# Performance work log

Hardware: AMD Instinct MI355X
Metric: run time of the kernel (lower is better)

Reference implementation:

```python
import jax, jax.numpy as jnp
import numpy as np

D_MODEL = 1024
H = 16
D_K = D_MODEL // H
D_FF = 4096
EPS = 1e-6


def setup_inputs() -> dict:
    key = jax.random.key(0)
    ks = jax.random.split(key, 12)
    B, S = 8, 1024
    s = 0.02
    inp = {
        "x": jax.random.normal(ks[0], (B, S, D_MODEL), dtype=jnp.float32),
        "src_mask": jnp.ones((B, 1, 1, S), dtype=jnp.int32),
        "wq": jax.random.normal(ks[1], (D_MODEL, D_MODEL), dtype=jnp.float32) * s,
        "bq": jnp.zeros((D_MODEL,), jnp.float32),
        "wk": jax.random.normal(ks[2], (D_MODEL, D_MODEL), dtype=jnp.float32) * s,
        "bk": jnp.zeros((D_MODEL,), jnp.float32),
        "wv": jax.random.normal(ks[3], (D_MODEL, D_MODEL), dtype=jnp.float32) * s,
        "bv": jnp.zeros((D_MODEL,), jnp.float32),
        "wo": jax.random.normal(ks[4], (D_MODEL, D_MODEL), dtype=jnp.float32) * s,
        "bo": jnp.zeros((D_MODEL,), jnp.float32),
        "w1": jax.random.normal(ks[5], (D_FF, D_MODEL), dtype=jnp.float32) * s,
        "b1": jnp.zeros((D_FF,), jnp.float32),
        "w2": jax.random.normal(ks[6], (D_MODEL, D_FF), dtype=jnp.float32) * s,
        "b2": jnp.zeros((D_MODEL,), jnp.float32),
        "ln1_a": jnp.ones((1,), jnp.float32),
        "ln1_b": jnp.zeros((1,), jnp.float32),
        "ln2_a": jnp.ones((1,), jnp.float32),
        "ln2_b": jnp.zeros((1,), jnp.float32),
    }
    return inp


def _layernorm(x, alpha, bias):
    # matches torch: std with Bessel correction (ddof=1), eps added to std
    mean = jnp.mean(x, axis=-1, keepdims=True)
    std = jnp.std(x, axis=-1, keepdims=True, ddof=1)
    return (x - mean) / (std + EPS) * alpha + bias


def reference(x, src_mask, wq, bq, wk, bk, wv, bv, wo, bo, w1, b1, w2, b2,
              ln1_a, ln1_b, ln2_a, ln2_b):
    B, S, _ = x.shape
    # --- residual 1: self attention on pre-normed x ---
    n = _layernorm(x, ln1_a, ln1_b)
    q = n @ wq.T + bq
    # NOTE: the source has a bug: key and value are views of the *query*
    # projection (w_k/w_v outputs are computed but discarded). We reproduce it.
    _ = n @ wk.T + bk
    _ = n @ wv.T + bv
    qh = q.reshape(B, S, H, D_K).transpose(0, 2, 1, 3)  # [B,H,S,dk]
    kh = qh
    vh = qh
    scores = jnp.einsum('bhqd,bhkd->bhqk', qh, kh) / jnp.sqrt(jnp.float32(D_K))
    scores = jnp.where(src_mask == 0, jnp.float32(-1e9), scores)
    attn = jax.nn.softmax(scores, axis=-1)
    ctx = jnp.einsum('bhqk,bhkd->bhqd', attn, vh)
    ctx = ctx.transpose(0, 2, 1, 3).reshape(B, S, D_MODEL)
    x = x + (ctx @ wo.T + bo)
    # --- residual 2: feed-forward (intended ReLU MLP) ---
    n2 = _layernorm(x, ln2_a, ln2_b)
    h = jax.nn.relu(n2 @ w1.T + b1)
    x = x + (h @ w2.T + b2)
    return x
```

## Files before the change

### kernel.cpp

```cpp
#include <hip/hip_runtime.h>
#include <hip/hip_bf16.h>

typedef __attribute__((ext_vector_type(8))) short short8;
typedef __attribute__((ext_vector_type(4))) float f32x4;

#define MFMA16(a, b, c) __builtin_amdgcn_mfma_f32_16x16x32_bf16((a), (b), (c), 0, 0, 0)

__device__ __forceinline__ unsigned short f2bf(float f) {
  union { float f; unsigned int u; } v; v.f = f;
  return (unsigned short)((v.u + 0x7fffu + ((v.u >> 16) & 1u)) >> 16);
}

__device__ __forceinline__ void gload_lds16(const void* g, void* l) {
  __builtin_amdgcn_global_load_lds((__attribute__((address_space(1))) void*)g,
                                   (__attribute__((address_space(3))) void*)l,
                                   16, 0, 0);
}

struct CvtArgs {
  const float* s0; const float* s1; const float* s2; const float* s3;
  unsigned short* d0; unsigned short* d1; unsigned short* d2; unsigned short* d3;
};

__global__ __launch_bounds__(256) void cvt_weights(CvtArgs a) {
  const long N0 = 1048576, N1 = 1048576, N2 = 4194304;
  long i = ((long)blockIdx.x * 256 + threadIdx.x) * 4;
  const float* s; unsigned short* d; long off;
  if (i < N0)                { s = a.s0; d = a.d0; off = i; }
  else if (i < N0 + N1)      { s = a.s1; d = a.d1; off = i - N0; }
  else if (i < N0 + N1 + N2) { s = a.s2; d = a.d2; off = i - N0 - N1; }
  else                       { s = a.s3; d = a.d3; off = i - N0 - N1 - N2; }
  float4 v = *(const float4*)(s + off);
  ushort4 o;
  o.x = f2bf(v.x); o.y = f2bf(v.y); o.z = f2bf(v.z); o.w = f2bf(v.w);
  *(ushort4*)(d + off) = o;
}

__global__ __launch_bounds__(256) void ln_kernel(
    const float* __restrict__ x,
    const float* __restrict__ alpha, const float* __restrict__ beta,
    unsigned short* __restrict__ out) {
  const int row = blockIdx.x;
  const int tid = threadIdx.x;
  const float4 v = ((const float4*)(x + (size_t)row * 1024))[tid];
  float s  = v.x + v.y + v.z + v.w;
  float sq = v.x * v.x + v.y * v.y + v.z * v.z + v.w * v.w;
  #pragma unroll
  for (int d = 32; d >= 1; d >>= 1) {
    s  += __shfl_xor(s, d, 64);
    sq += __shfl_xor(sq, d, 64);
  }
  __shared__ float red[8];
  const int w = tid >> 6;
  if ((tid & 63) == 0) { red[w] = s; red[4 + w] = sq; }
  __syncthreads();
  s  = red[0] + red[1] + red[2] + red[3];
  sq = red[4] + red[5] + red[6] + red[7];
  const float mean = s * (1.f / 1024.f);
  float var = (sq - s * mean) * (1.f / 1023.f);
  var = fmaxf(var, 0.f);
  const float rs = alpha[0] / (sqrtf(var) + 1e-6f);
  const float bb = beta[0];
  ushort4 o;
  o.x = f2bf((v.x - mean) * rs + bb);
  o.y = f2bf((v.y - mean) * rs + bb);
  o.z = f2bf((v.z - mean) * rs + bb);
  o.w = f2bf((v.w - mean) * rs + bb);
  ((ushort4*)out)[(size_t)row * 256 + tid] = o;
}

template <int OUT_BF16, int RELU, int NF, int WQT, int DBUF>
__global__ __launch_bounds__(512, 2) void gemm2ph(
    const unsigned short* __restrict__ A, int lda,
    const unsigned short* __restrict__ B, int ldb,
    const float* __restrict__ bias,
    const float* __restrict__ residual,
    void* __restrict__ Cout,
    unsigned short* __restrict__ qTout,
    int M, int N, int K, float cscale, int nbx) {
  constexpr int STG = DBUF ? (32768 + NF * 8192) : (16384 + NF * 4096);
  constexpr int EPI = OUT_BF16 ? 128 * (NF * 64 + 4) : 256 * (NF * 64 + 4);
  constexpr int LSH = STG > EPI ? STG : EPI;
  __shared__ __align__(16) unsigned short lds[LSH];
  const int NT = K >> 6;
  const int tid = threadIdx.x;
  const int w = tid >> 6, lane = tid & 63;
  const int cpx = gridDim.x >> 3;
  const int id = (blockIdx.x & 7) * cpx + (blockIdx.x >> 3);
  const int bx = id % nbx, by = id / nbx;
  const int row0 = by * 256, col0 = bx * (NF * 64);
  const int wr128 = (w >> 2) * 128, wcN = (w & 3) * (NF * 16);
  const int lq = lane & 15, g = lane >> 4, g4 = g * 4;
  const int strow = tid >> 3;
  const int sunit8 = ((tid & 7) ^ (strow & 7)) * 8;

  const unsigned short* Asrc = A + (size_t)(row0 + strow) * lda + sunit8;
  const unsigned short* Bsrc = B + (size_t)(col0 + strow) * ldb + sunit8;

  auto stage = [&](int buf, int tt) {
    unsigned short* Ad = lds + (DBUF ? buf * 16384 : 0) + w * 512;
    unsigned short* Bd = lds + (DBUF ? 32768 + buf * (NF * 4096) : 16384) + w * 512;
    #pragma unroll
    for (int c = 0; c < 4; ++c)
      gload_lds16(Asrc + (size_t)(c * 64) * lda + tt * 64, Ad + c * 4096);
    #pragma unroll
    for (int c = 0; c < NF; ++c)
      gload_lds16(Bsrc + (size_t)(c * 64) * ldb + tt * 64, Bd + c * 4096);
  };

  f32x4 acc[8][NF] = {};

  auto compute = [&](int buf) {
    const unsigned short* Ab = lds + (DBUF ? buf * 16384 : 0);
    const unsigned short* Bb = lds + (DBUF ? 32768 + buf * (NF * 4096) : 16384);
    #pragma unroll
    for (int kk = 0; kk < 2; ++kk) {
      short8 af[8], bf[NF];
      #pragma unroll
      for (int m = 0; m < 8; ++m) {
        const int r = wr128 + m * 16 + lq;
        af[m] = *(const short8*)(Ab + r * 64 + (((kk * 4 + g) ^ (r & 7)) << 3));
      }
      #pragma unroll
      for (int n = 0; n < NF; ++n) {
        const int r = wcN + n * 16 + lq;
        bf[n] = *(const short8*)(Bb + r * 64 + (((kk * 4 + g) ^ (r & 7)) << 3));
      }
      __builtin_amdgcn_s_setprio(1);
      #pragma unroll
      for (int m = 0; m < 8; ++m)
        #pragma unroll
        for (int n = 0; n < NF; ++n)
          acc[m][n] = MFMA16(af[m], bf[n], acc[m][n]);
      __builtin_amdgcn_s_setprio(0);
    }
  };

  if (DBUF) {
    stage(0, 0);
    asm volatile("s_waitcnt vmcnt(0)" ::: "memory");
    __builtin_amdgcn_s_barrier();
    int buf = 0;
    for (int t = 0; t < NT; ++t) {
      if (t + 1 < NT) stage(buf ^ 1, t + 1);
      compute(buf);
      if (t + 1 < NT) {
        asm volatile("s_waitcnt vmcnt(0)" ::: "memory");
        __builtin_amdgcn_s_barrier();
        buf ^= 1;
      }
    }
  } else {
    for (int t = 0; t < NT; ++t) {
      __syncthreads();
      stage(0, t);
      asm volatile("s_waitcnt vmcnt(0)" ::: "memory");
      __syncthreads();
      compute(0);
    }
  }

  float bv[NF];
  #pragma unroll
  for (int n = 0; n < NF; ++n) bv[n] = bias[col0 + wcN + n * 16 + lq];

  if (OUT_BF16) {
    const int CW = NF * 64 + 4;
    unsigned short* cbuf = lds;
    __syncthreads();
    #pragma unroll
    for (int p = 0; p < 2; ++p) {
      if ((w >> 2) == p) {
        #pragma unroll
        for (int m = 0; m < 8; ++m)
          #pragma unroll
          for (int n = 0; n < NF; ++n)
            #pragma unroll
            for (int r = 0; r < 4; ++r) {
              float v = (acc[m][n][r] + bv[n]) * cscale;
              if (RELU) v = fmaxf(v, 0.f);
              cbuf[(m * 16 + g4 + r) * CW + wcN + n * 16 + lq] = f2bf(v);
            }
      }
      __syncthreads();
      #pragma unroll
      for (int i = 0; i < 2 * NF; ++i) {
        const int un = i * 512 + tid;
        const int row = un / (8 * NF);
        const int cu = un % (8 * NF);
        const short8 vv = *(const short8*)&cbuf[row * CW + cu * 8];
        *(short8*)((unsigned short*)Cout + (size_t)(row0 + p * 128 + row) * N + col0 + cu * 8) = vv;
      }
      if (WQT) {
        const int grow = row0 + p * 128;
        const int bb = grow >> 10;
        const int s0 = grow & 1023;
        const int h0 = col0 >> 6;
        #pragma unroll
        for (int i = 0; i < 4; ++i) {
          const int un = i * 512 + tid;
          const int colx = un >> 4;
          const int su = un & 15;
          const int hh = h0 + (colx >> 6);
          const int dd = colx & 63;
          short8 o;
          #pragma unroll
          for (int j = 0; j < 8; ++j) o[j] = (short)cbuf[(su * 8 + j) * CW + colx];
          *(short8*)(qTout + ((size_t)(bb * 16 + hh) * 64 + dd) * 1024 + s0 + su * 8) = o;
        }
      }
      __syncthreads();
    }
  } else {
    const int CWf = NF * 64 + 4;
    float* cbuf = (float*)lds;
    __syncthreads();
    #pragma unroll
    for (int p = 0; p < 2; ++p) {
      if ((w >> 2) == p) {
        #pragma unroll
        for (int m = 0; m < 8; ++m)
          #pragma unroll
          for (int n = 0; n < NF; ++n)
            #pragma unroll
            for (int r = 0; r < 4; ++r) {
              float v = (acc[m][n][r] + bv[n]) * cscale;
              if (RELU) v = fmaxf(v, 0.f);
              cbuf[(m * 16 + g4 + r) * CWf + wcN + n * 16 + lq] = v;
            }
      }
      __syncthreads();
      #pragma unroll
      for (int i = 0; i < 4 * NF; ++i) {
        const int un = i * 512 + tid;
        const int row = un / (16 * NF);
        const int cu = un % (16 * NF);
        float4 v = *(const float4*)&cbuf[row * CWf + cu * 4];
        const size_t idx = (size_t)(row0 + p * 128 + row) * N + col0 + cu * 4;
        if (residual) {
          const float4 rv = *(const float4*)(residual + idx);
          v.x += rv.x; v.y += rv.y; v.z += rv.z; v.w += rv.w;
        }
        *(float4*)((float*)Cout + idx) = v;
      }
      __syncthreads();
    }
  }
}

__global__ __launch_bounds__(256) void attn_kernel(
    const unsigned short* __restrict__ q,
    const unsigned short* __restrict__ qT,
    const int* __restrict__ mask,
    unsigned short* __restrict__ ctx) {
  __shared__ __align__(16) unsigned short Ks[2][64 * 64];
  __shared__ __align__(16) unsigned short Vs[2][64 * 64];
  __shared__ int allmask;
  const int id = blockIdx.x;
  const int bh = ((id & 7) << 4) + (id >> 6);
  const int qt = (id >> 3) & 7;
  const int b = bh >> 4, h = bh & 15;
  const int tid = threadIdx.x, w = tid >> 6, lane = tid & 63;
  const int lq = lane & 15;
  const int g = lane >> 4;
  const int lk8 = g * 8;
  const int swz = lane & 7;
  const int q0 = qt * 128 + w * 32;
  const size_t qbase = (size_t)b * (1024 * 1024) + h * 64;
  const size_t qTb = (size_t)bh * 64 * 1024;
  const int srow = lane >> 3;
  const int su = (lane & 7) ^ srow;
  const size_t ksrc = qbase + (size_t)(w * 16 + srow) * 1024 + su * 8;
  const size_t vsrc = qTb + (size_t)(w * 16 + srow) * 1024 + su * 8;
  const float RS = 2.3548202f;

  auto stage = [&](int bufi, int kt) {
    char* Kd = (char*)Ks[bufi] + w * 2048;
    char* Vd = (char*)Vs[bufi] + w * 2048;
    gload_lds16(q + ksrc + (size_t)(kt * 64) * 1024, Kd);
    gload_lds16(q + ksrc + (size_t)(kt * 64 + 8) * 1024, Kd + 1024);
    gload_lds16(qT + vsrc + kt * 64, Vd);
    gload_lds16(qT + vsrc + (size_t)8 * 1024 + kt * 64, Vd + 1024);
  };

  const int* mrow = mask + b * 1024;
  if (tid == 0) allmask = 1;
  int mp = 1;
  #pragma unroll
  for (int i = 0; i < 4; ++i) mp &= (mrow[tid + i * 256] != 0);
  stage(0, 0);
  __syncthreads();
  if (!__all(mp) && lane == 0) atomicAnd(&allmask, 0);
  asm volatile("s_waitcnt vmcnt(0)" ::: "memory");
  __syncthreads();
  const bool fullmask = (allmask != 0);

  short8 qa[2][2];
  #pragma unroll
  for (int qf = 0; qf < 2; ++qf)
    #pragma unroll
    for (int kk = 0; kk < 2; ++kk)
      qa[qf][kk] = *(const short8*)&q[qbase + (size_t)(q0 + qf * 16 + lq) * 1024 + kk * 32 + lk8];

  short8 ones;
  #pragma unroll
  for (int i = 0; i < 8; ++i) ones[i] = (short)0x3F80;

  f32x4 lacc[2] = {};
  f32x4 Oa[2][4];
  #pragma unroll
  for (int mf = 0; mf < 2; ++mf)
    #pragma unroll
    for (int nf = 0; nf < 4; ++nf) Oa[mf][nf] = (f32x4){0.f, 0.f, 0.f, 0.f};

  int cur = 0;

  for (int kt = 0; kt < 16; ++kt) {
    const int k0 = kt * 64;
    if (kt < 15) stage(cur ^ 1, kt + 1);
    const char* Kb = (const char*)Ks[cur];
    const char* Vb = (const char*)Vs[cur];
    f32x4 s[2][4];
    #pragma unroll
    for (int qf = 0; qf < 2; ++qf)
      #pragma unroll
      for (int kf = 0; kf < 4; ++kf) s[qf][kf] = (f32x4){0.f, 0.f, 0.f, 0.f};
    #pragma unroll
    for (int kf = 0; kf < 4; ++kf) {
      const char* kr = Kb + (kf * 16 + lq) * 128;
      const short8 ka0 = *(const short8*)(kr + (((g) ^ swz) << 4));
      const short8 ka1 = *(const short8*)(kr + (((4 + g) ^ swz) << 4));
      s[0][kf] = MFMA16(ka0, qa[0][0], s[0][kf]);
      s[0][kf] = MFMA16(ka1, qa[0][1], s[0][kf]);
      s[1][kf] = MFMA16(ka0, qa[1][0], s[1][kf]);
      s[1][kf] = MFMA16(ka1, qa[1][1], s[1][kf]);
    }
    if (!fullmask) {
      #pragma unroll
      for (int kf = 0; kf < 4; ++kf) {
        const int4 mv = *(const int4*)&mrow[k0 + kf * 16 + g * 4];
        float madd[4];
        madd[0] = mv.x ? 0.f : -1e9f; madd[1] = mv.y ? 0.f : -1e9f;
        madd[2] = mv.z ? 0.f : -1e9f; madd[3] = mv.w ? 0.f : -1e9f;
        #pragma unroll
        for (int qf = 0; qf < 2; ++qf)
          #pragma unroll
          for (int r = 0; r < 4; ++r)
            s[qf][kf][r] += madd[r];
      }
    }
    unsigned int E[2][4], O[2][4];
    #pragma unroll
    for (int qf = 0; qf < 2; ++qf) {
      #pragma unroll
      for (int kf = 0; kf < 4; ++kf) {
        float p0 = exp2f(s[qf][kf][0]);
        float p1 = exp2f(s[qf][kf][1]);
        float p2 = exp2f(s[qf][kf][2]);
        float p3 = exp2f(s[qf][kf][3]);
        asm("v_cvt_pk_bf16_f32 %0, %1, %2" : "=v"(E[qf][kf]) : "v"(p0), "v"(p1));
        asm("v_cvt_pk_bf16_f32 %0, %1, %2" : "=v"(O[qf][kf]) : "v"(p2), "v"(p3));
      }
    }
    short8 pa[2][2];
    #pragma unroll
    for (int qf = 0; qf < 2; ++qf) {
      #pragma unroll
      for (int ks = 0; ks < 2; ++ks) {
        unsigned int e0 = E[qf][2 * ks], e1 = E[qf][2 * ks + 1];
        unsigned int o0 = O[qf][2 * ks], o1 = O[qf][2 * ks + 1];
        asm("v_permlane32_swap_b32 %0, %1" : "+v"(e0), "+v"(e1));
        asm("v_permlane16_swap_b32 %0, %1" : "+v"(e0), "+v"(e1));
        asm("v_permlane32_swap_b32 %0, %1" : "+v"(o0), "+v"(o1));
        asm("v_permlane16_swap_b32 %0, %1" : "+v"(o0), "+v"(o1));
        union { unsigned int u[4]; short8 s8; } pw;
        pw.u[0] = e0; pw.u[1] = o0; pw.u[2] = e1; pw.u[3] = o1;
        pa[qf][ks] = pw.s8;
      }
    }
    #pragma unroll
    for (int ks = 0; ks < 2; ++ks) {
      #pragma unroll
      for (int nf = 0; nf < 4; ++nf) {
        const short8 vb = *(const short8*)(Vb + (nf * 16 + lq) * 128 + (((4 * ks + g) ^ swz) << 4));
        Oa[0][nf] = MFMA16(pa[0][ks], vb, Oa[0][nf]);
        Oa[1][nf] = MFMA16(pa[1][ks], vb, Oa[1][nf]);
      }
      lacc[0] = MFMA16(pa[0][ks], ones, lacc[0]);
      lacc[1] = MFMA16(pa[1][ks], ones, lacc[1]);
    }
    __syncthreads();
    cur ^= 1;
  }
  #pragma unroll
  for (int mf = 0; mf < 2; ++mf) {
    #pragma unroll
    for (int r = 0; r < 4; ++r) {
      const float linv = RS / lacc[mf][r];
      const int row = q0 + mf * 16 + g * 4 + r;
      #pragma unroll
      for (int nf = 0; nf < 4; ++nf) {
        const int col = h * 64 + nf * 16 + lq;
        ctx[((size_t)b * 1024 + row) * 1024 + col] = f2bf(Oa[mf][nf][r] * linv);
      }
    }
  }
}

extern "C" void kernel_launch(void* const* d_in, const int* in_sizes, int n_in,
                              void* d_out, int out_size, void* d_ws, size_t ws_size,
                              hipStream_t stream) {
  const float* x    = (const float*)d_in[0];
  const int*   mask = (const int*)d_in[1];
  const float* wq   = (const float*)d_in[2];
  const float* bq   = (const float*)d_in[3];
  const float* wo   = (const float*)d_in[8];
  const float* bo   = (const float*)d_in[9];
  const float* w1   = (const float*)d_in[10];
  const float* b1   = (const float*)d_in[11];
  const float* w2   = (const float*)d_in[12];
  const float* b2   = (const float*)d_in[13];
  const float* ln1a = (const float*)d_in[14];
  const float* ln1b = (const float*)d_in[15];
  const float* ln2a = (const float*)d_in[16];
  const float* ln2b = (const float*)d_in[17];
  float* out = (float*)d_out;

  char* ws = (char*)d_ws;
  unsigned short* wq_b  = (unsigned short*)(ws);
  unsigned short* wo_b  = (unsigned short*)(ws + (2l << 20));
  unsigned short* w1_b  = (unsigned short*)(ws + (4l << 20));
  unsigned short* w2_b  = (unsigned short*)(ws + (12l << 20));
  unsigned short* n_b   = (unsigned short*)(ws + (20l << 20));
  unsigned short* q_b   = (unsigned short*)(ws + (36l << 20));
  unsigned short* qT_b  = (unsigned short*)(ws + (52l << 20));
  unsigned short* ctx_b = (unsigned short*)(ws + (68l << 20));
  unsigned short* h_b   = (unsigned short*)(ws + (84l << 20));

  const float SQRT_SC = 0.42466090f;

  CvtArgs ca{wq, wo, w1, w2, wq_b, wo_b, w1_b, w2_b};
  cvt_weights<<<10240, 256, 0, stream>>>(ca);
  ln_kernel<<<8192, 256, 0, stream>>>(x, ln1a, ln1b, n_b);
  gemm2ph<1, 0, 2, 1, 1><<<256, 512, 0, stream>>>(n_b, 1024, wq_b, 1024, bq, nullptr, q_b, qT_b, 8192, 1024, 1024, SQRT_SC, 8);
  attn_kernel<<<1024, 256, 0, stream>>>(q_b, qT_b, mask, ctx_b);
  gemm2ph<0, 0, 2, 0, 1><<<256, 512, 0, stream>>>(ctx_b, 1024, wo_b, 1024, bo, x, out, nullptr, 8192, 1024, 1024, 1.0f, 8);
  ln_kernel<<<8192, 256, 0, stream>>>(out, ln2a, ln2b, n_b);
  gemm2ph<1, 1, 4, 0, 1><<<512, 512, 0, stream>>>(n_b, 1024, w1_b, 1024, b1, nullptr, h_b, nullptr, 8192, 4096, 1024, 1.0f, 16);
  gemm2ph<0, 0, 2, 0, 1><<<256, 512, 0, stream>>>(h_b, 4096, w2_b, 4096, b2, out, out, nullptr, 8192, 1024, 4096, 1.0f, 8);
}
```

Before: 296.8 us.

## Fuse weight conversion with first layernorm and enlarge attention blocks to 256 queries

Merges the bf16 weight-conversion kernel and the first layernorm into one launch, with blocks dispatched by index range, which removes one kernel launch and its tail. The attention kernel now runs 512 threads (8 waves) per block, each block covering 256 query rows instead of 128. The K/V tiles staged to LDS are therefore shared by twice as many waves, halving per-block staging loads and the grid size. Fewer blocks (512) may reduce occupancy balance across CUs.

```diff
diff --git a/kernel.cpp b/kernel.cpp
--- a/kernel.cpp
+++ b/kernel.cpp
@@ -22,18 +22,52 @@
   unsigned short* d0; unsigned short* d1; unsigned short* d2; unsigned short* d3;
 };
 
-__global__ __launch_bounds__(256) void cvt_weights(CvtArgs a) {
-  const long N0 = 1048576, N1 = 1048576, N2 = 4194304;
-  long i = ((long)blockIdx.x * 256 + threadIdx.x) * 4;
-  const float* s; unsigned short* d; long off;
-  if (i < N0)                { s = a.s0; d = a.d0; off = i; }
-  else if (i < N0 + N1)      { s = a.s1; d = a.d1; off = i - N0; }
-  else if (i < N0 + N1 + N2) { s = a.s2; d = a.d2; off = i - N0 - N1; }
-  else                       { s = a.s3; d = a.d3; off = i - N0 - N1 - N2; }
-  float4 v = *(const float4*)(s + off);
-  ushort4 o;
-  o.x = f2bf(v.x); o.y = f2bf(v.y); o.z = f2bf(v.z); o.w = f2bf(v.w);
-  *(ushort4*)(d + off) = o;
+__global__ __launch_bounds__(256) void cvt_ln(
+    CvtArgs a,
+    const float* __restrict__ x,
+    const float* __restrict__ alpha, const float* __restrict__ beta,
+    unsigned short* __restrict__ out) {
+  const int tid = threadIdx.x;
+  if (blockIdx.x < 8192) {
+    const int row = blockIdx.x;
+    const float4 v = ((const float4*)(x + (size_t)row * 1024))[tid];
+    float s  = v.x + v.y + v.z + v.w;
+    float sq = v.x * v.x + v.y * v.y + v.z * v.z + v.w * v.w;
+    #pragma unroll
+    for (int d = 32; d >= 1; d >>= 1) {
+      s  += __shfl_xor(s, d, 64);
+      sq += __shfl_xor(sq, d, 64);
+    }
+    __shared__ float red[8];
+    const int w = tid >> 6;
+    if ((tid & 63) == 0) { red[w] = s; red[4 + w] = sq; }
+    __syncthreads();
+    s  = red[0] + red[1] + red[2] + red[3];
+    sq = red[4] + red[5] + red[6] + red[7];
+    const float mean = s * (1.f / 1024.f);
+    float var = (sq - s * mean) * (1.f / 1023.f);
+    var = fmaxf(var, 0.f);
+    const float rs = alpha[0] / (sqrtf(var) + 1e-6f);
+    const float bb = beta[0];
+    ushort4 o;
+    o.x = f2bf((v.x - mean) * rs + bb);
+    o.y = f2bf((v.y - mean) * rs + bb);
+    o.z = f2bf((v.z - mean) * rs + bb);
+    o.w = f2bf((v.w - mean) * rs + bb);
+    ((ushort4*)out)[(size_t)row * 256 + tid] = o;
+  } else {
+    const long N0 = 1048576, N1 = 1048576, N2 = 4194304;
+    long i = ((long)(blockIdx.x - 8192) * 256 + tid) * 4;
+    const float* s; unsigned short* d; long off;
+    if (i < N0)                { s = a.s0; d = a.d0; off = i; }
+    else if (i < N0 + N1)      { s = a.s1; d = a.d1; off = i - N0; }
+    else if (i < N0 + N1 + N2) { s = a.s2; d = a.d2; off = i - N0 - N1; }
+    else                       { s = a.s3; d = a.d3; off = i - N0 - N1 - N2; }
+    float4 v = *(const float4*)(s + off);
+    ushort4 o;
+    o.x = f2bf(v.x); o.y = f2bf(v.y); o.z = f2bf(v.z); o.w = f2bf(v.w);
+    *(ushort4*)(d + off) = o;
+  }
 }
 
 __global__ __launch_bounds__(256) void ln_kernel(
@@ -248,7 +282,7 @@
   }
 }
 
-__global__ __launch_bounds__(256) void attn_kernel(
+__global__ __launch_bounds__(512) void attn_kernel(
     const unsigned short* __restrict__ q,
     const unsigned short* __restrict__ qT,
     const int* __restrict__ mask,
@@ -257,37 +291,33 @@
   __shared__ __align__(16) unsigned short Vs[2][64 * 64];
   __shared__ int allmask;
   const int id = blockIdx.x;
-  const int bh = ((id & 7) << 4) + (id >> 6);
-  const int qt = (id >> 3) & 7;
+  const int bh = ((id & 7) << 4) + (id >> 5);
+  const int qt = (id >> 3) & 3;
   const int b = bh >> 4, h = bh & 15;
   const int tid = threadIdx.x, w = tid >> 6, lane = tid & 63;
   const int lq = lane & 15;
   const int g = lane >> 4;
   const int lk8 = g * 8;
   const int swz = lane & 7;
-  const int q0 = qt * 128 + w * 32;
+  const int q0 = qt * 256 + w * 32;
   const size_t qbase = (size_t)b * (1024 * 1024) + h * 64;
   const size_t qTb = (size_t)bh * 64 * 1024;
   const int srow = lane >> 3;
   const int su = (lane & 7) ^ srow;
-  const size_t ksrc = qbase + (size_t)(w * 16 + srow) * 1024 + su * 8;
-  const size_t vsrc = qTb + (size_t)(w * 16 + srow) * 1024 + su * 8;
+  const size_t ksrc = qbase + (size_t)(w * 8 + srow) * 1024 + su * 8;
+  const size_t vsrc = qTb + (size_t)(w * 8 + srow) * 1024 + su * 8;
   const float RS = 2.3548202f;
 
   auto stage = [&](int bufi, int kt) {
-    char* Kd = (char*)Ks[bufi] + w * 2048;
-    char* Vd = (char*)Vs[bufi] + w * 2048;
-    gload_lds16(q + ksrc + (size_t)(kt * 64) * 1024, Kd);
-    gload_lds16(q + ksrc + (size_t)(kt * 64 + 8) * 1024, Kd + 1024);
-    gload_lds16(qT + vsrc + kt * 64, Vd);
-    gload_lds16(qT + vsrc + (size_t)8 * 1024 + kt * 64, Vd + 1024);
+    gload_lds16(q + ksrc + (size_t)(kt * 64) * 1024, (char*)Ks[bufi] + w * 1024);
+    gload_lds16(qT + vsrc + kt * 64, (char*)Vs[bufi] + w * 1024);
   };
 
   const int* mrow = mask + b * 1024;
   if (tid == 0) allmask = 1;
   int mp = 1;
   #pragma unroll
-  for (int i = 0; i < 4; ++i) mp &= (mrow[tid + i * 256] != 0);
+  for (int i = 0; i < 2; ++i) mp &= (mrow[tid + i * 512] != 0);
   stage(0, 0);
   __syncthreads();
   if (!__all(mp) && lane == 0) atomicAnd(&allmask, 0);
@@ -440,10 +470,9 @@
   const float SQRT_SC = 0.42466090f;
 
   CvtArgs ca{wq, wo, w1, w2, wq_b, wo_b, w1_b, w2_b};
-  cvt_weights<<<10240, 256, 0, stream>>>(ca);
-  ln_kernel<<<8192, 256, 0, stream>>>(x, ln1a, ln1b, n_b);
+  cvt_ln<<<18432, 256, 0, stream>>>(ca, x, ln1a, ln1b, n_b);
   gemm2ph<1, 0, 2, 1, 1><<<256, 512, 0, stream>>>(n_b, 1024, wq_b, 1024, bq, nullptr, q_b, qT_b, 8192, 1024, 1024, SQRT_SC, 8);
-  attn_kernel<<<1024, 256, 0, stream>>>(q_b, qT_b, mask, ctx_b);
+  attn_kernel<<<512, 512, 0, stream>>>(q_b, qT_b, mask, ctx_b);
   gemm2ph<0, 0, 2, 0, 1><<<256, 512, 0, stream>>>(ctx_b, 1024, wo_b, 1024, bo, x, out, nullptr, 8192, 1024, 1024, 1.0f, 8);
   ln_kernel<<<8192, 256, 0, stream>>>(out, ln2a, ln2b, n_b);
   gemm2ph<1, 1, 4, 0, 1><<<512, 512, 0, stream>>>(n_b, 1024, w1_b, 1024, b1, nullptr, h_b, nullptr, 8192, 4096, 1024, 1.0f, 16);
```

Result: faster. 278.6 us (-6.2%).
